# Performance work log

Hardware: AMD Instinct MI355X
Metric: run time of the kernel (lower is better)

## Reference

```python
import jax, jax.numpy as jnp
import numpy as np

INPUT_SIZE = 32
UNITS = 1024
T = 8192
N_MODULES = 2
INPUT_SCALING = 1.0
SPECTRAL_RADIUS = 0.99
LEAKY = 0.5
C_IN = 10
C_REC = 10


def _sparse_input_kernel(rng, M, N, C):
    # each row (input dim) projects to C random reservoir units, U(-1,1)
    W = np.zeros((M, N), dtype=np.float32)
    for i in range(M):
        idx = rng.choice(N, size=C, replace=False)
        W[i, idx] = rng.uniform(-1.0, 1.0, size=C).astype(np.float32)
    return W


def _sparse_recurrent_kernel(rng, M, C):
    # each column (unit) receives input from C random units, U(-1,1)
    W = np.zeros((M, M), dtype=np.float32)
    for i in range(M):
        idx = rng.choice(M, size=C, replace=False)
        W[idx, i] = rng.uniform(-1.0, 1.0, size=C).astype(np.float32)
    return W


def _make_recurrent(rng, M, leaky, rho):
    W = _sparse_recurrent_kernel(rng, M, C_REC)
    I = np.eye(M, dtype=np.float32)
    if leaky == 1:
        e = np.linalg.eigvals(W)
        W = W * (rho / np.max(np.abs(e)))
    else:
        W = W * leaky + I * (1.0 - leaky)
        e = np.linalg.eigvals(W)
        W = W * (rho / np.max(np.abs(e)))
        W = (W + I * (leaky - 1.0)) * (1.0 / leaky)
    return W.astype(np.float32)


def setup_inputs() -> dict:
    key = jax.random.key(0)
    rng = np.random.default_rng(0)
    u = jax.random.normal(key, (1, T, INPUT_SIZE), dtype=jnp.float32)
    # module 0: input_size -> units; module 1: units -> units
    kernel0 = jnp.asarray(_sparse_input_kernel(rng, INPUT_SIZE, UNITS, C_IN) * INPUT_SCALING)
    rec0 = jnp.asarray(_make_recurrent(rng, UNITS, LEAKY, SPECTRAL_RADIUS))
    bias0 = jnp.asarray(rng.uniform(-1.0, 1.0, size=UNITS).astype(np.float32))
    kernel1 = jnp.asarray(_sparse_input_kernel(rng, UNITS, UNITS, C_IN) * INPUT_SCALING)
    rec1 = jnp.asarray(_make_recurrent(rng, UNITS, LEAKY, SPECTRAL_RADIUS))
    bias1 = jnp.asarray(rng.uniform(-1.0, 1.0, size=UNITS).astype(np.float32))
    return {"u": u, "kernel0": kernel0, "rec0": rec0, "bias0": bias0,
            "kernel1": kernel1, "rec1": rec1, "bias1": bias1}


def _run_reservoir(u, K, W, b):
    # u: [B, T, in]; leaky-integrator ESN scan over time
    def step(h, ut):
        out = jnp.tanh(ut @ K + b + h @ W)
        h_new = h * (1.0 - LEAKY) + out * LEAKY
        return h_new, h_new
    h0 = jnp.zeros((u.shape[0], K.shape[1]), dtype=u.dtype)
    _, hs = jax.lax.scan(step, h0, jnp.swapaxes(u, 0, 1))  # [T, B, units]
    return jnp.swapaxes(hs, 0, 1)  # [B, T, units]


def reference(u, kernel0, rec0, bias0, kernel1, rec1, bias1):
    hs0 = _run_reservoir(u, kernel0, rec0, bias0)
    hs1 = _run_reservoir(hs0, kernel1, rec1, bias1)
    # deep reservoir output: concatenation of all module state sequences
    return jnp.concatenate([hs0, hs1], axis=-1)  # [1, T, 2*UNITS]
```

## Files before the change

kernel.cpp:

```cpp
#include <hip/hip_runtime.h>
#include <math.h>

typedef unsigned int uint;
typedef unsigned short ushort_t;

#define T_STEPS 8192
#define UNITS 1024
#define REC_CAP 10
#define K1_CAP 32
#define K0_CAP 8

__global__ __launch_bounds__(256) void prep_kernel(
    const float* __restrict__ k0w, const float* __restrict__ r0w,
    const float* __restrict__ r1w, const float* __restrict__ k1w,
    float* __restrict__ rec_val, ushort_t* __restrict__ rec_idx,
    float* __restrict__ rec_diag,
    float* __restrict__ k1_val, ushort_t* __restrict__ k1_idx,
    int* __restrict__ k1_cnt,
    float* __restrict__ k0_val, ushort_t* __restrict__ k0_idx,
    int* __restrict__ k0_cnt)
{
    int tid = blockIdx.x * blockDim.x + threadIdx.x;
    int task = tid >> 10;
    int j = tid & 1023;

    if (task == 0 || task == 1) {
        const float* W = (task == 0) ? r0w : r1w;
        float diag = 0.0f;
        int c = 0;
        int base = (task * 1024 + j) * REC_CAP;
        for (int i = 0; i < 1024; ++i) {
            float v = W[i * 1024 + j];
            if (i == j) { diag = v; }
            else if (v != 0.0f && c < REC_CAP) {
                rec_val[base + c] = v;
                rec_idx[base + c] = (ushort_t)(i * 4);
                ++c;
            }
        }
        for (; c < REC_CAP; ++c) { rec_val[base + c] = 0.0f; rec_idx[base + c] = 0; }
        rec_diag[task * 1024 + j] = diag;
    } else if (task == 2) {
        int c = 0;
        int base = j * K1_CAP;
        for (int i = 0; i < 1024; ++i) {
            float v = k1w[i * 1024 + j];
            if (v != 0.0f && c < K1_CAP) {
                k1_val[base + c] = v;
                k1_idx[base + c] = (ushort_t)(i * 4);
                ++c;
            }
        }
        k1_cnt[j] = c;
        for (; c < K1_CAP; ++c) { k1_val[base + c] = 0.0f; k1_idx[base + c] = 0; }
    } else if (task == 3) {
        int c = 0;
        int base = j * K0_CAP;
        for (int i = 0; i < 32; ++i) {
            float v = k0w[i * 1024 + j];
            if (v != 0.0f && c < K0_CAP) {
                k0_val[base + c] = v;
                k0_idx[base + c] = (ushort_t)(i * 4);
                ++c;
            }
        }
        k0_cnt[j] = c;
        for (; c < K0_CAP; ++c) { k0_val[base + c] = 0.0f; k0_idx[base + c] = 0; }
    }
}

__device__ __forceinline__ float fast_tanh(float x) {
    float ax = fabsf(x);
    float e  = __expf(-2.0f * ax);
    float r  = __builtin_amdgcn_rcpf(1.0f + e);
    float t  = (1.0f - e) * r;
    return copysignf(t, x);
}

#define STEP(P, tt)                                                            \
  {                                                                            \
    const char* h0rd = (const char*)(&hbuf[(P)][0]);                           \
    float x0 = b0 + d0 * h0j;                                                  \
    _Pragma("unroll")                                                          \
    for (int k = 0; k < REC_CAP; ++k) {                                        \
      uint off = (k & 1) ? (r0o[k >> 1] >> 16) : (r0o[k >> 1] & 0xffffu);      \
      x0 += r0v[k] * *(const float*)(h0rd + off);                              \
    }                                                                          \
    const char* urd = (const char*)u_lds + (((tt) & 63) << 7);                 \
    _Pragma("unroll")                                                          \
    for (int kc = 0; kc < K0_CAP; kc += 2) {                                   \
      if (kc < k0m) {                                                          \
        _Pragma("unroll")                                                      \
        for (int k = kc; k < kc + 2; ++k) {                                    \
          uint off = (k & 1) ? (k0o[k >> 1] >> 16) : (k0o[k >> 1] & 0xffffu);  \
          x0 += k0v[k] * *(const float*)(urd + off);                           \
        }                                                                      \
      }                                                                        \
    }                                                                          \
    float o0  = fast_tanh(x0);                                                 \
    float h0n = 0.5f * (h0j + o0);                                             \
    out[(tt) * 2048 + j] = h0n;                                                \
    hbuf[1 - (P)][j] = h0n;                                                    \
    __syncthreads();                                                           \
    float x1 = b1 + d1 * h1j;                                                  \
    const char* h0nrd = (const char*)(&hbuf[1 - (P)][0]);                      \
    _Pragma("unroll")                                                          \
    for (int kc = 0; kc < K1_CAP; kc += 4) {                                   \
      if (kc < k1m) {                                                          \
        _Pragma("unroll")                                                      \
        for (int k = kc; k < kc + 4; ++k) {                                    \
          uint off = (k & 1) ? (k1o[k >> 1] >> 16) : (k1o[k >> 1] & 0xffffu);  \
          x1 += k1v[k] * *(const float*)(h0nrd + off);                         \
        }                                                                      \
      }                                                                        \
    }                                                                          \
    const char* h1rd = (const char*)(&hbuf[2 + (P)][0]);                       \
    _Pragma("unroll")                                                          \
    for (int k = 0; k < REC_CAP; ++k) {                                        \
      uint off = (k & 1) ? (r1o[k >> 1] >> 16) : (r1o[k >> 1] & 0xffffu);      \
      x1 += r1v[k] * *(const float*)(h1rd + off);                              \
    }                                                                          \
    float o1  = fast_tanh(x1);                                                 \
    float h1n = 0.5f * (h1j + o1);                                             \
    out[(tt) * 2048 + 1024 + j] = h1n;                                         \
    hbuf[2 + (1 - (P))][j] = h1n;                                              \
    __syncthreads();                                                           \
    h0j = h0n;                                                                 \
    h1j = h1n;                                                                 \
  }

__global__ __launch_bounds__(1024) void reservoir_main(
    const float* __restrict__ u,
    const float* __restrict__ bias0, const float* __restrict__ bias1,
    const float* __restrict__ rec_val, const ushort_t* __restrict__ rec_idx,
    const float* __restrict__ rec_diag,
    const float* __restrict__ k1_val, const ushort_t* __restrict__ k1_idx,
    const int* __restrict__ k1_cnt,
    const float* __restrict__ k0_val, const ushort_t* __restrict__ k0_idx,
    const int* __restrict__ k0_cnt,
    float* __restrict__ out)
{
    __shared__ float hbuf[4][UNITS];
    __shared__ float u_lds[2048];
    const int j = threadIdx.x;

    float r0v[REC_CAP], r1v[REC_CAP], k1v[K1_CAP], k0v[K0_CAP];
    uint  r0o[REC_CAP / 2], r1o[REC_CAP / 2], k1o[K1_CAP / 2], k0o[K0_CAP / 2];
#pragma unroll
    for (int k = 0; k < REC_CAP; ++k) {
        r0v[k] = rec_val[j * REC_CAP + k];
        r1v[k] = rec_val[(1024 + j) * REC_CAP + k];
    }
    {
        const uint* p0 = (const uint*)(rec_idx + j * REC_CAP);
        const uint* p1 = (const uint*)(rec_idx + (1024 + j) * REC_CAP);
#pragma unroll
        for (int k = 0; k < REC_CAP / 2; ++k) { r0o[k] = p0[k]; r1o[k] = p1[k]; }
    }
#pragma unroll
    for (int k = 0; k < K1_CAP; ++k) k1v[k] = k1_val[j * K1_CAP + k];
    {
        const uint* p = (const uint*)(k1_idx + j * K1_CAP);
#pragma unroll
        for (int k = 0; k < K1_CAP / 2; ++k) k1o[k] = p[k];
    }
#pragma unroll
    for (int k = 0; k < K0_CAP; ++k) k0v[k] = k0_val[j * K0_CAP + k];
    {
        const uint* p = (const uint*)(k0_idx + j * K0_CAP);
#pragma unroll
        for (int k = 0; k < K0_CAP / 2; ++k) k0o[k] = p[k];
    }
    const float b0  = bias0[j], b1 = bias1[j];
    const float d0  = rec_diag[j], d1 = rec_diag[1024 + j];

    int k1m = k1_cnt[j];
    int k0m = k0_cnt[j];
#pragma unroll
    for (int s = 32; s >= 1; s >>= 1) {
        int o1v = __shfl_xor(k1m, s, 64);
        k1m = (o1v > k1m) ? o1v : k1m;
        int o0v = __shfl_xor(k0m, s, 64);
        k0m = (o0v > k0m) ? o0v : k0m;
    }
    k1m = __builtin_amdgcn_readfirstlane(k1m);
    k0m = __builtin_amdgcn_readfirstlane(k0m);

    hbuf[0][j] = 0.0f; hbuf[1][j] = 0.0f; hbuf[2][j] = 0.0f; hbuf[3][j] = 0.0f;
    float h0j = 0.0f, h1j = 0.0f;

    for (int t = 0; t < T_STEPS; t += 2) {
        if ((t & 63) == 0) {
            u_lds[j]        = u[t * 32 + j];
            u_lds[1024 + j] = u[t * 32 + 1024 + j];
            __syncthreads();
        }
        STEP(0, t)
        STEP(1, t + 1)
    }
}

extern "C" void kernel_launch(void* const* d_in, const int* in_sizes, int n_in,
                              void* d_out, int out_size, void* d_ws, size_t ws_size,
                              hipStream_t stream) {
    const float* u   = (const float*)d_in[0];
    const float* k0w = (const float*)d_in[1];
    const float* r0w = (const float*)d_in[2];
    const float* b0  = (const float*)d_in[3];
    const float* k1w = (const float*)d_in[4];
    const float* r1w = (const float*)d_in[5];
    const float* b1  = (const float*)d_in[6];
    float* out = (float*)d_out;

    char* w = (char*)d_ws;
    float* rec_val  = (float*)w;  w += 2 * 1024 * REC_CAP * sizeof(float);
    float* rec_diag = (float*)w;  w += 2 * 1024 * sizeof(float);
    float* k1_val   = (float*)w;  w += 1024 * K1_CAP * sizeof(float);
    float* k0_val   = (float*)w;  w += 1024 * K0_CAP * sizeof(float);
    ushort_t* rec_idx = (ushort_t*)w; w += 2 * 1024 * REC_CAP * sizeof(ushort_t);
    ushort_t* k1_idx  = (ushort_t*)w; w += 1024 * K1_CAP * sizeof(ushort_t);
    ushort_t* k0_idx  = (ushort_t*)w; w += 1024 * K0_CAP * sizeof(ushort_t);
    int* k1_cnt = (int*)w;        w += 1024 * sizeof(int);
    int* k0_cnt = (int*)w;

    prep_kernel<<<16, 256, 0, stream>>>(k0w, r0w, r1w, k1w,
                                        rec_val, rec_idx, rec_diag,
                                        k1_val, k1_idx, k1_cnt,
                                        k0_val, k0_idx, k0_cnt);

    reservoir_main<<<1, 1024, 0, stream>>>(u, b0, b1,
                                           rec_val, rec_idx, rec_diag,
                                           k1_val, k1_idx, k1_cnt,
                                           k0_val, k0_idx, k0_cnt,
                                           out);
}
```

Measured before the change: 16.37 ms.

## Reorder units by fan-in, sort gather addresses per lane, drop a barrier per step

Adds a second prep kernel that permutes reservoir units so each wavefront holds units with similar nonzero counts. This shrinks the per-wave maximum loop trip count. Each thread's gather addresses are reordered by bank relative to its lane to reduce LDS bank conflicts. The main loop keeps one __syncthreads per timestep instead of two, relying on double-buffered state, and splits each dot product into two accumulators for more ILP. Output writes now go through a permutation pointer. The cost is an extra serial prep launch and more complex index bookkeeping.

Result: slower. 22.72 ms (+38.8%).

```diff
diff --git a/kernel.cpp b/kernel.cpp
--- a/kernel.cpp
+++ b/kernel.cpp
@@ -2,70 +2,153 @@
 #include <math.h>
 
 typedef unsigned int uint;
-typedef unsigned short ushort_t;
 
 #define T_STEPS 8192
-#define UNITS 1024
-#define REC_CAP 10
+#define R_CAP 10
 #define K1_CAP 32
 #define K0_CAP 8
 
-__global__ __launch_bounds__(256) void prep_kernel(
+__global__ __launch_bounds__(256) void prep_extract(
     const float* __restrict__ k0w, const float* __restrict__ r0w,
     const float* __restrict__ r1w, const float* __restrict__ k1w,
-    float* __restrict__ rec_val, ushort_t* __restrict__ rec_idx,
-    float* __restrict__ rec_diag,
-    float* __restrict__ k1_val, ushort_t* __restrict__ k1_idx,
-    int* __restrict__ k1_cnt,
-    float* __restrict__ k0_val, ushort_t* __restrict__ k0_idx,
-    int* __restrict__ k0_cnt)
+    float* __restrict__ r0vr, uint* __restrict__ r0ur, float* __restrict__ d0r,
+    float* __restrict__ r1vr, uint* __restrict__ r1ur, float* __restrict__ d1r,
+    float* __restrict__ k1vr, uint* __restrict__ k1ur, int* __restrict__ c1r,
+    float* __restrict__ k0vr, uint* __restrict__ k0ur, int* __restrict__ c0r)
 {
-    int tid = blockIdx.x * blockDim.x + threadIdx.x;
-    int task = tid >> 10;
-    int j = tid & 1023;
-
-    if (task == 0 || task == 1) {
-        const float* W = (task == 0) ? r0w : r1w;
-        float diag = 0.0f;
-        int c = 0;
-        int base = (task * 1024 + j) * REC_CAP;
+    int tid = blockIdx.x * 256 + threadIdx.x;
+    int task = tid >> 10, j = tid & 1023;
+
+    if (task <= 1) {
+        const float* W = task ? r1w : r0w;
+        float* vr = task ? r1vr : r0vr;
+        uint*  ur = task ? r1ur : r0ur;
+        float* dr = task ? d1r  : d0r;
+        float diag = 0.f; int c = 0;
+#pragma unroll 4
         for (int i = 0; i < 1024; ++i) {
             float v = W[i * 1024 + j];
-            if (i == j) { diag = v; }
-            else if (v != 0.0f && c < REC_CAP) {
-                rec_val[base + c] = v;
-                rec_idx[base + c] = (ushort_t)(i * 4);
-                ++c;
+            if (i == j) diag = v;
+            else if (v != 0.f && c < R_CAP) {
+                vr[j * R_CAP + c] = v; ur[j * R_CAP + c] = (uint)i; ++c;
             }
         }
-        for (; c < REC_CAP; ++c) { rec_val[base + c] = 0.0f; rec_idx[base + c] = 0; }
-        rec_diag[task * 1024 + j] = diag;
+        for (; c < R_CAP; ++c) { vr[j * R_CAP + c] = 0.f; ur[j * R_CAP + c] = 0u; }
+        dr[j] = diag;
     } else if (task == 2) {
         int c = 0;
-        int base = j * K1_CAP;
+#pragma unroll 4
         for (int i = 0; i < 1024; ++i) {
             float v = k1w[i * 1024 + j];
-            if (v != 0.0f && c < K1_CAP) {
-                k1_val[base + c] = v;
-                k1_idx[base + c] = (ushort_t)(i * 4);
-                ++c;
+            if (v != 0.f && c < K1_CAP) {
+                k1vr[j * K1_CAP + c] = v; k1ur[j * K1_CAP + c] = (uint)i; ++c;
             }
         }
-        k1_cnt[j] = c;
-        for (; c < K1_CAP; ++c) { k1_val[base + c] = 0.0f; k1_idx[base + c] = 0; }
-    } else if (task == 3) {
+        c1r[j] = c;
+        for (int q = c; q < K1_CAP; ++q) { k1vr[j * K1_CAP + q] = 0.f; k1ur[j * K1_CAP + q] = 0u; }
+    } else {
         int c = 0;
-        int base = j * K0_CAP;
         for (int i = 0; i < 32; ++i) {
             float v = k0w[i * 1024 + j];
-            if (v != 0.0f && c < K0_CAP) {
-                k0_val[base + c] = v;
-                k0_idx[base + c] = (ushort_t)(i * 4);
-                ++c;
+            if (v != 0.f && c < K0_CAP) {
+                k0vr[j * K0_CAP + c] = v; k0ur[j * K0_CAP + c] = (uint)i; ++c;
             }
         }
-        k0_cnt[j] = c;
-        for (; c < K0_CAP; ++c) { k0_val[base + c] = 0.0f; k0_idx[base + c] = 0; }
+        c0r[j] = c;
+        for (int q = c; q < K0_CAP; ++q) { k0vr[j * K0_CAP + q] = 0.f; k0ur[j * K0_CAP + q] = 0u; }
+    }
+}
+
+__device__ void sort_pack(const float* ev, const uint* ea, int n, int cap,
+                          int lane, float* vout, uint* aout)
+{
+    float sv[K1_CAP]; uint sa[K1_CAP];
+    uint used = 0;
+    for (int k = 0; k < n; ++k) {
+        int best = 0, bkey = 1000;
+        for (int m = 0; m < n; ++m) if (!((used >> m) & 1)) {
+            int key = (int)(((ea[m] >> 2) - (uint)lane) & 31u);
+            if (key < bkey) { bkey = key; best = m; }
+        }
+        used |= 1u << best;
+        sv[k] = ev[best]; sa[k] = ea[best];
+    }
+    for (int k = n; k < cap; ++k) { sv[k] = ev[k]; sa[k] = ea[k]; }
+    for (int k = 0; k < cap; ++k) vout[k] = sv[k];
+    for (int p = 0; p < cap / 2; ++p) aout[p] = (sa[2 * p] & 0xffffu) | (sa[2 * p + 1] << 16);
+}
+
+__global__ __launch_bounds__(1024) void prep_pack(
+    const float* __restrict__ r0vr, const uint* __restrict__ r0ur,
+    const float* __restrict__ r1vr, const uint* __restrict__ r1ur,
+    const float* __restrict__ k1vr, const uint* __restrict__ k1ur, const int* __restrict__ c1r,
+    const float* __restrict__ k0vr, const uint* __restrict__ k0ur, const int* __restrict__ c0r,
+    float* __restrict__ F_r0v, uint* __restrict__ F_r0a,
+    float* __restrict__ F_r1v, uint* __restrict__ F_r1a,
+    float* __restrict__ F_k1v, uint* __restrict__ F_k1a,
+    float* __restrict__ F_k0v, uint* __restrict__ F_k0a,
+    int* __restrict__ F_c1, int* __restrict__ F_c0,
+    int* __restrict__ F_u0, int* __restrict__ F_u1)
+{
+    __shared__ int lc1[1024], lc0[1024];
+    __shared__ unsigned short linv0[1024], linv1[1024];
+    const int j = threadIdx.x;
+    const int c1j = c1r[j], c0j = c0r[j];
+    lc1[j] = c1j; lc0[j] = c0j;
+    __syncthreads();
+    int s1 = 0, s0 = 0;
+#pragma unroll 4
+    for (int i = 0; i < 1024; ++i) {
+        int a = lc1[i]; s1 += (a < c1j) || (a == c1j && i < j);
+        int b = lc0[i]; s0 += (b < c0j) || (b == c0j && i < j);
+    }
+    linv0[j] = (unsigned short)s0;
+    linv1[j] = (unsigned short)s1;
+    __syncthreads();
+
+    {
+        const int lane = s0 & 63;
+        float ev[R_CAP]; uint ea[R_CAP]; int n = 0;
+        for (int k = 0; k < R_CAP; ++k) {
+            float v = r0vr[j * R_CAP + k];
+            uint  u = r0ur[j * R_CAP + k];
+            ev[k] = v;
+            ea[k] = (v != 0.f) ? ((uint)linv0[u] << 2) : 0u;
+            if (v != 0.f) n = k + 1;
+        }
+        sort_pack(ev, ea, n, R_CAP, lane, F_r0v + s0 * R_CAP, F_r0a + s0 * (R_CAP / 2));
+
+        float kv[K0_CAP]; uint ka[K0_CAP];
+        int c = c0j;
+        for (int k = 0; k < K0_CAP; ++k) {
+            kv[k] = k0vr[j * K0_CAP + k];
+            ka[k] = (k < c) ? (k0ur[j * K0_CAP + k] << 2) : 0u;
+        }
+        sort_pack(kv, ka, c, K0_CAP, lane, F_k0v + s0 * K0_CAP, F_k0a + s0 * (K0_CAP / 2));
+        F_c0[s0] = c0j;
+        F_u0[s0] = j;
+    }
+    {
+        const int lane = s1 & 63;
+        float ev[R_CAP]; uint ea[R_CAP]; int n = 0;
+        for (int k = 0; k < R_CAP; ++k) {
+            float v = r1vr[j * R_CAP + k];
+            uint  u = r1ur[j * R_CAP + k];
+            ev[k] = v;
+            ea[k] = (v != 0.f) ? (8192u + ((uint)linv1[u] << 2)) : 8192u;
+            if (v != 0.f) n = k + 1;
+        }
+        sort_pack(ev, ea, n, R_CAP, lane, F_r1v + s1 * R_CAP, F_r1a + s1 * (R_CAP / 2));
+
+        float kv[K1_CAP]; uint ka[K1_CAP];
+        int c = c1j;
+        for (int k = 0; k < K1_CAP; ++k) {
+            kv[k] = k1vr[j * K1_CAP + k];
+            ka[k] = (k < c) ? ((uint)linv0[k1ur[j * K1_CAP + k]] << 2) : 0u;
+        }
+        sort_pack(kv, ka, c, K1_CAP, lane, F_k1v + s1 * K1_CAP, F_k1a + s1 * (K1_CAP / 2));
+        F_c1[s1] = c1j;
+        F_u1[s1] = j;
     }
 }
 
@@ -77,126 +160,112 @@
     return copysignf(t, x);
 }
 
-#define STEP(P, tt)                                                            \
+#define LD(A) (*(const float*)(smem + (A)))
+
+#define STEP(P, UOFF)                                                          \
   {                                                                            \
-    const char* h0rd = (const char*)(&hbuf[(P)][0]);                           \
-    float x0 = b0 + d0 * h0j;                                                  \
+    float xa = __builtin_fmaf(d0, h0j, b0), xb = 0.f;                          \
     _Pragma("unroll")                                                          \
-    for (int k = 0; k < REC_CAP; ++k) {                                        \
-      uint off = (k & 1) ? (r0o[k >> 1] >> 16) : (r0o[k >> 1] & 0xffffu);      \
-      x0 += r0v[k] * *(const float*)(h0rd + off);                              \
+    for (int k = 0; k < R_CAP; k += 2) {                                       \
+      uint pr = r0a[k >> 1];                                                   \
+      xa += r0v[k]     * LD((pr & 0xffffu) + (P) * 4096);                      \
+      xb += r0v[k + 1] * LD((pr >> 16)     + (P) * 4096);                      \
     }                                                                          \
-    const char* urd = (const char*)u_lds + (((tt) & 63) << 7);                 \
     _Pragma("unroll")                                                          \
     for (int kc = 0; kc < K0_CAP; kc += 2) {                                   \
       if (kc < k0m) {                                                          \
-        _Pragma("unroll")                                                      \
-        for (int k = kc; k < kc + 2; ++k) {                                    \
-          uint off = (k & 1) ? (k0o[k >> 1] >> 16) : (k0o[k >> 1] & 0xffffu);  \
-          x0 += k0v[k] * *(const float*)(urd + off);                           \
-        }                                                                      \
+        uint pr = k0a[kc >> 1];                                                \
+        xa += k0v[kc]     * LD((pr & 0xffffu) + (UOFF));                       \
+        xb += k0v[kc + 1] * LD((pr >> 16)     + (UOFF));                       \
       }                                                                        \
     }                                                                          \
-    float o0  = fast_tanh(x0);                                                 \
+    float o0  = fast_tanh(xa + xb);                                            \
     float h0n = 0.5f * (h0j + o0);                                             \
-    out[(tt) * 2048 + j] = h0n;                                                \
-    hbuf[1 - (P)][j] = h0n;                                                    \
+    ((float*)(smem + (1 - (P)) * 4096))[j] = h0n;                              \
+    o0g[0] = h0n; o0g += 2048;                                                 \
     __syncthreads();                                                           \
-    float x1 = b1 + d1 * h1j;                                                  \
-    const char* h0nrd = (const char*)(&hbuf[1 - (P)][0]);                      \
+    float ya = __builtin_fmaf(d1, h1j, b1), yb = 0.f;                          \
     _Pragma("unroll")                                                          \
-    for (int kc = 0; kc < K1_CAP; kc += 4) {                                   \
+    for (int kc = 0; kc < K1_CAP; kc += 2) {                                   \
       if (kc < k1m) {                                                          \
-        _Pragma("unroll")                                                      \
-        for (int k = kc; k < kc + 4; ++k) {                                    \
-          uint off = (k & 1) ? (k1o[k >> 1] >> 16) : (k1o[k >> 1] & 0xffffu);  \
-          x1 += k1v[k] * *(const float*)(h0nrd + off);                         \
-        }                                                                      \
+        uint pr = k1a[kc >> 1];                                                \
+        ya += k1v[kc]     * LD((pr & 0xffffu) + (1 - (P)) * 4096);             \
+        yb += k1v[kc + 1] * LD((pr >> 16)     + (1 - (P)) * 4096);             \
       }                                                                        \
     }                                                                          \
-    const char* h1rd = (const char*)(&hbuf[2 + (P)][0]);                       \
     _Pragma("unroll")                                                          \
-    for (int k = 0; k < REC_CAP; ++k) {                                        \
-      uint off = (k & 1) ? (r1o[k >> 1] >> 16) : (r1o[k >> 1] & 0xffffu);      \
-      x1 += r1v[k] * *(const float*)(h1rd + off);                              \
+    for (int k = 0; k < R_CAP; k += 2) {                                       \
+      uint pr = r1a[k >> 1];                                                   \
+      ya += r1v[k]     * LD((pr & 0xffffu) + (P) * 4096);                      \
+      yb += r1v[k + 1] * LD((pr >> 16)     + (P) * 4096);                      \
     }                                                                          \
-    float o1  = fast_tanh(x1);                                                 \
+    float o1  = fast_tanh(ya + yb);                                            \
     float h1n = 0.5f * (h1j + o1);                                             \
-    out[(tt) * 2048 + 1024 + j] = h1n;                                         \
-    hbuf[2 + (1 - (P))][j] = h1n;                                              \
-    __syncthreads();                                                           \
-    h0j = h0n;                                                                 \
-    h1j = h1n;                                                                 \
+    ((float*)(smem + 8192 + (1 - (P)) * 4096))[j] = h1n;                       \
+    o1g[0] = h1n; o1g += 2048;                                                 \
+    h0j = h0n; h1j = h1n;                                                      \
   }
 
 __global__ __launch_bounds__(1024) void reservoir_main(
     const float* __restrict__ u,
     const float* __restrict__ bias0, const float* __restrict__ bias1,
-    const float* __restrict__ rec_val, const ushort_t* __restrict__ rec_idx,
-    const float* __restrict__ rec_diag,
-    const float* __restrict__ k1_val, const ushort_t* __restrict__ k1_idx,
-    const int* __restrict__ k1_cnt,
-    const float* __restrict__ k0_val, const ushort_t* __restrict__ k0_idx,
-    const int* __restrict__ k0_cnt,
+    const float* __restrict__ d0r, const float* __restrict__ d1r,
+    const float* __restrict__ F_r0v, const uint* __restrict__ F_r0a,
+    const float* __restrict__ F_r1v, const uint* __restrict__ F_r1a,
+    const float* __restrict__ F_k1v, const uint* __restrict__ F_k1a,
+    const float* __restrict__ F_k0v, const uint* __restrict__ F_k0a,
+    const int* __restrict__ F_c1, const int* __restrict__ F_c0,
+    const int* __restrict__ F_u0, const int* __restrict__ F_u1,
     float* __restrict__ out)
 {
-    __shared__ float hbuf[4][UNITS];
-    __shared__ float u_lds[2048];
+    __shared__ __align__(16) char smem[24576];
     const int j = threadIdx.x;
 
-    float r0v[REC_CAP], r1v[REC_CAP], k1v[K1_CAP], k0v[K0_CAP];
-    uint  r0o[REC_CAP / 2], r1o[REC_CAP / 2], k1o[K1_CAP / 2], k0o[K0_CAP / 2];
-#pragma unroll
-    for (int k = 0; k < REC_CAP; ++k) {
-        r0v[k] = rec_val[j * REC_CAP + k];
-        r1v[k] = rec_val[(1024 + j) * REC_CAP + k];
-    }
-    {
-        const uint* p0 = (const uint*)(rec_idx + j * REC_CAP);
-        const uint* p1 = (const uint*)(rec_idx + (1024 + j) * REC_CAP);
-#pragma unroll
-        for (int k = 0; k < REC_CAP / 2; ++k) { r0o[k] = p0[k]; r1o[k] = p1[k]; }
-    }
-#pragma unroll
-    for (int k = 0; k < K1_CAP; ++k) k1v[k] = k1_val[j * K1_CAP + k];
-    {
-        const uint* p = (const uint*)(k1_idx + j * K1_CAP);
-#pragma unroll
-        for (int k = 0; k < K1_CAP / 2; ++k) k1o[k] = p[k];
-    }
-#pragma unroll
-    for (int k = 0; k < K0_CAP; ++k) k0v[k] = k0_val[j * K0_CAP + k];
-    {
-        const uint* p = (const uint*)(k0_idx + j * K0_CAP);
-#pragma unroll
-        for (int k = 0; k < K0_CAP / 2; ++k) k0o[k] = p[k];
-    }
-    const float b0  = bias0[j], b1 = bias1[j];
-    const float d0  = rec_diag[j], d1 = rec_diag[1024 + j];
-
-    int k1m = k1_cnt[j];
-    int k0m = k0_cnt[j];
+    float r0v[R_CAP], r1v[R_CAP], k1v[K1_CAP], k0v[K0_CAP];
+    uint  r0a[R_CAP / 2], r1a[R_CAP / 2], k1a[K1_CAP / 2], k0a[K0_CAP / 2];
+#pragma unroll
+    for (int k = 0; k < R_CAP; ++k) { r0v[k] = F_r0v[j * R_CAP + k]; r1v[k] = F_r1v[j * R_CAP + k]; }
+#pragma unroll
+    for (int k = 0; k < R_CAP / 2; ++k) { r0a[k] = F_r0a[j * (R_CAP / 2) + k]; r1a[k] = F_r1a[j * (R_CAP / 2) + k]; }
+#pragma unroll
+    for (int k = 0; k < K1_CAP; ++k) k1v[k] = F_k1v[j * K1_CAP + k];
+#pragma unroll
+    for (int k = 0; k < K1_CAP / 2; ++k) k1a[k] = F_k1a[j * (K1_CAP / 2) + k];
+#pragma unroll
+    for (int k = 0; k < K0_CAP; ++k) k0v[k] = F_k0v[j * K0_CAP + k];
+#pragma unroll
+    for (int k = 0; k < K0_CAP / 2; ++k) k0a[k] = F_k0a[j * (K0_CAP / 2) + k];
+
+    const int u0 = F_u0[j], u1 = F_u1[j];
+    const float b0 = bias0[u0], d0 = d0r[u0];
+    const float b1 = bias1[u1], d1 = d1r[u1];
+    float* o0g = out + u0;
+    float* o1g = out + 1024 + u1;
+
+    int k1m = F_c1[j], k0m = F_c0[j];
 #pragma unroll
     for (int s = 32; s >= 1; s >>= 1) {
-        int o1v = __shfl_xor(k1m, s, 64);
-        k1m = (o1v > k1m) ? o1v : k1m;
-        int o0v = __shfl_xor(k0m, s, 64);
-        k0m = (o0v > k0m) ? o0v : k0m;
+        int a = __shfl_xor(k1m, s, 64); k1m = a > k1m ? a : k1m;
+        int b = __shfl_xor(k0m, s, 64); k0m = b > k0m ? b : k0m;
     }
     k1m = __builtin_amdgcn_readfirstlane(k1m);
     k0m = __builtin_amdgcn_readfirstlane(k0m);
 
-    hbuf[0][j] = 0.0f; hbuf[1][j] = 0.0f; hbuf[2][j] = 0.0f; hbuf[3][j] = 0.0f;
-    float h0j = 0.0f, h1j = 0.0f;
+    ((float*)(smem        ))[j] = 0.f;
+    ((float*)(smem +  4096))[j] = 0.f;
+    ((float*)(smem +  8192))[j] = 0.f;
+    ((float*)(smem + 12288))[j] = 0.f;
+    float h0j = 0.f, h1j = 0.f;
 
     for (int t = 0; t < T_STEPS; t += 2) {
         if ((t & 63) == 0) {
-            u_lds[j]        = u[t * 32 + j];
-            u_lds[1024 + j] = u[t * 32 + 1024 + j];
+            ((float*)(smem + 16384))[j]        = u[t * 32 + j];
+            ((float*)(smem + 16384))[1024 + j] = u[t * 32 + 1024 + j];
             __syncthreads();
         }
-        STEP(0, t)
-        STEP(1, t + 1)
+        uint uoff = 16384u + (uint)((t & 63) << 7);
+        STEP(0, uoff)
+        STEP(1, uoff + 128u)
     }
 }
 
@@ -213,24 +282,41 @@
     float* out = (float*)d_out;
 
     char* w = (char*)d_ws;
-    float* rec_val  = (float*)w;  w += 2 * 1024 * REC_CAP * sizeof(float);
-    float* rec_diag = (float*)w;  w += 2 * 1024 * sizeof(float);
-    float* k1_val   = (float*)w;  w += 1024 * K1_CAP * sizeof(float);
-    float* k0_val   = (float*)w;  w += 1024 * K0_CAP * sizeof(float);
-    ushort_t* rec_idx = (ushort_t*)w; w += 2 * 1024 * REC_CAP * sizeof(ushort_t);
-    ushort_t* k1_idx  = (ushort_t*)w; w += 1024 * K1_CAP * sizeof(ushort_t);
-    ushort_t* k0_idx  = (ushort_t*)w; w += 1024 * K0_CAP * sizeof(ushort_t);
-    int* k1_cnt = (int*)w;        w += 1024 * sizeof(int);
-    int* k0_cnt = (int*)w;
-
-    prep_kernel<<<16, 256, 0, stream>>>(k0w, r0w, r1w, k1w,
-                                        rec_val, rec_idx, rec_diag,
-                                        k1_val, k1_idx, k1_cnt,
-                                        k0_val, k0_idx, k0_cnt);
-
-    reservoir_main<<<1, 1024, 0, stream>>>(u, b0, b1,
-                                           rec_val, rec_idx, rec_diag,
-                                           k1_val, k1_idx, k1_cnt,
-                                           k0_val, k0_idx, k0_cnt,
-                                           out);
-}
+    float* r0vr = (float*)w; w += 1024 * R_CAP * 4;
+    uint*  r0ur = (uint*)w;  w += 1024 * R_CAP * 4;
+    float* d0r  = (float*)w; w += 1024 * 4;
+    float* r1vr = (float*)w; w += 1024 * R_CAP * 4;
+    uint*  r1ur = (uint*)w;  w += 1024 * R_CAP * 4;
+    float* d1r  = (float*)w; w += 1024 * 4;
+    float* k1vr = (float*)w; w += 1024 * K1_CAP * 4;
+    uint*  k1ur = (uint*)w;  w += 1024 * K1_CAP * 4;
+    int*   c1r  = (int*)w;   w += 1024 * 4;
+    float* k0vr = (float*)w; w += 1024 * K0_CAP * 4;
+    uint*  k0ur = (uint*)w;  w += 1024 * K0_CAP * 4;
+    int*   c0r  = (int*)w;   w += 1024 * 4;
+    float* F_r0v = (float*)w; w += 1024 * R_CAP * 4;
+    uint*  F_r0a = (uint*)w;  w += 1024 * (R_CAP / 2) * 4;
+    float* F_r1v = (float*)w; w += 1024 * R_CAP * 4;
+    uint*  F_r1a = (uint*)w;  w += 1024 * (R_CAP / 2) * 4;
+    float* F_k1v = (float*)w; w += 1024 * K1_CAP * 4;
+    uint*  F_k1a = (uint*)w;  w += 1024 * (K1_CAP / 2) * 4;
+    float* F_k0v = (float*)w; w += 1024 * K0_CAP * 4;
+    uint*  F_k0a = (uint*)w;  w += 1024 * (K0_CAP / 2) * 4;
+    int*   F_c1 = (int*)w;   w += 1024 * 4;
+    int*   F_c0 = (int*)w;   w += 1024 * 4;
+    int*   F_u0 = (int*)w;   w += 1024 * 4;
+    int*   F_u1 = (int*)w;
+
+    prep_extract<<<16, 256, 0, stream>>>(k0w, r0w, r1w, k1w,
+                                         r0vr, r0ur, d0r, r1vr, r1ur, d1r,
+                                         k1vr, k1ur, c1r, k0vr, k0ur, c0r);
+    prep_pack<<<1, 1024, 0, stream>>>(r0vr, r0ur, r1vr, r1ur,
+                                      k1vr, k1ur, c1r, k0vr, k0ur, c0r,
+                                      F_r0v, F_r0a, F_r1v, F_r1a,
+                                      F_k1v, F_k1a, F_k0v, F_k0a,
+                                      F_c1, F_c0, F_u0, F_u1);
+    reservoir_main<<<1, 1024, 0, stream>>>(u, b0, b1, d0r, d1r,
+                                           F_r0v, F_r0a, F_r1v, F_r1a,
+                                           F_k1v, F_k1a, F_k0v, F_k0a,
+                                           F_c1, F_c0, F_u0, F_u1, out);
+}
```
